# Kernel tuning notes

Hardware: AMD Instinct MI355X
Metric: run time of the kernel (lower is better)

The kernel has to match this reference:

```python
import jax, jax.numpy as jnp
import numpy as np

B, T, IN, H = 131072, 10, 1, 32


def setup_inputs() -> dict:
    key = jax.random.key(0)
    ks = jax.random.split(key, 8)
    s = 1.0 / np.sqrt(H)  # torch default uniform bound 1/sqrt(hidden)
    return {
        "x": jax.random.normal(ks[0], (B, T, IN), dtype=jnp.float32),
        "h_state": jnp.zeros((1, B, H), dtype=jnp.float32),
        "W_ih": jax.random.uniform(ks[1], (H, IN), jnp.float32, -s, s),
        "W_hh": jax.random.uniform(ks[2], (H, H), jnp.float32, -s, s),
        "b_ih": jax.random.uniform(ks[3], (H,), jnp.float32, -s, s),
        "b_hh": jax.random.uniform(ks[4], (H,), jnp.float32, -s, s),
        "W_out": jax.random.uniform(ks[5], (1, H), jnp.float32, -s, s),
        "b_out": jax.random.uniform(ks[6], (1,), jnp.float32, -s, s),
    }


def reference(x, h_state, W_ih, W_hh, b_ih, b_hh, W_out, b_out):
    # single-layer tanh RNN, batch_first; h_state: [1, B, H]
    h0 = h_state[0]  # [B, H]
    xs = jnp.swapaxes(x, 0, 1)  # [T, B, IN]

    def step(h, xt):
        h_new = jnp.tanh(xt @ W_ih.T + b_ih + h @ W_hh.T + b_hh)
        return h_new, h_new

    hT, hs = jax.lax.scan(step, h0, xs)  # hs: [T, B, H]
    r_out = jnp.swapaxes(hs, 0, 1)  # [B, T, H]
    outs = r_out @ W_out.T + b_out  # [B, T, 1] (same as view(-1,32)->Linear->view)
    return outs, hT[None]
```

## Files before the change

kernel.cpp:

```cpp
#include <hip/hip_runtime.h>

typedef __attribute__((ext_vector_type(4))) float f32x4;
typedef __attribute__((ext_vector_type(8))) short s16x8;
typedef __attribute__((ext_vector_type(4))) int   i32x4;

constexpr int BATCH = 131072;
constexpr int T = 10;
constexpr int H = 32;

__device__ __forceinline__ unsigned cvt_pk_bf16(float a, float b) {
    unsigned d;
    asm("v_cvt_pk_bf16_f32 %0, %1, %2" : "=v"(d) : "v"(a), "v"(b));
    return d;
}

__device__ __forceinline__ void pack_hilo8(const float (&v)[8], i32x4& hi, i32x4& lo) {
    #pragma unroll
    for (int p = 0; p < 4; ++p) {
        unsigned hb = cvt_pk_bf16(v[2*p], v[2*p+1]);
        float f0 = __builtin_bit_cast(float, hb << 16);
        float f1 = __builtin_bit_cast(float, hb & 0xFFFF0000u);
        hi[p] = (int)hb;
        lo[p] = (int)cvt_pk_bf16(v[2*p] - f0, v[2*p+1] - f1);
    }
}

__device__ __forceinline__ i32x4 pack_hi8(const float (&v)[8]) {
    i32x4 hi;
    #pragma unroll
    for (int p = 0; p < 4; ++p)
        hi[p] = (int)cvt_pk_bf16(v[2*p], v[2*p+1]);
    return hi;
}

__device__ __forceinline__ f32x4 mfma16(i32x4 a, i32x4 b, f32x4 c) {
    return __builtin_amdgcn_mfma_f32_16x16x32_bf16(
        __builtin_bit_cast(s16x8, a), __builtin_bit_cast(s16x8, b), c, 0, 0, 0);
}

__device__ __forceinline__ float fast_tanh(float v) {
    float e = __expf(2.0f * v);
    return fmaf(-2.0f, __builtin_amdgcn_rcpf(e + 1.0f), 1.0f);
}


extern "C" __global__ void __launch_bounds__(256, 4)
rnn_mfma(const float* __restrict__ x,
         const float* __restrict__ h0,
         const float* __restrict__ W_ih,
         const float* __restrict__ W_hh,
         const float* __restrict__ b_ih,
         const float* __restrict__ b_hh,
         const float* __restrict__ W_out,
         const float* __restrict__ b_out,
         float* __restrict__ out)
{
    const int tid  = threadIdx.x;
    const int wave = tid >> 6;
    const int lane = tid & 63;
    const int nl   = lane & 15;
    const int g    = lane >> 4;
    const int base = blockIdx.x * 128 + wave * 32;
    const int m0   = base + nl;
    const int m1   = base + 16 + nl;

    i32x4 a0h, a0l, a1h, a1l;
    {
        float v[8];
        const float* r0 = W_hh + nl * H;
        float4 u0 = *reinterpret_cast<const float4*>(r0 + 4 * g);
        float4 u1 = *reinterpret_cast<const float4*>(r0 + 16 + 4 * g);
        v[0]=u0.x; v[1]=u0.y; v[2]=u0.z; v[3]=u0.w;
        v[4]=u1.x; v[5]=u1.y; v[6]=u1.z; v[7]=u1.w;
        pack_hilo8(v, a0h, a0l);
        const float* r1 = W_hh + (nl + 16) * H;
        float4 w0 = *reinterpret_cast<const float4*>(r1 + 4 * g);
        float4 w1 = *reinterpret_cast<const float4*>(r1 + 16 + 4 * g);
        v[0]=w0.x; v[1]=w0.y; v[2]=w0.z; v[3]=w0.w;
        v[4]=w1.x; v[5]=w1.y; v[6]=w1.z; v[7]=w1.w;
        pack_hilo8(v, a1h, a1l);
    }

    float vb0[4], vw0[4], wo0[4], vb1[4], vw1[4], wo1[4];
    #pragma unroll
    for (int r = 0; r < 4; ++r) {
        const int j0 = 4 * g + r, j1 = j0 + 16;
        vb0[r] = b_ih[j0] + b_hh[j0]; vw0[r] = W_ih[j0]; wo0[r] = W_out[j0];
        vb1[r] = b_ih[j1] + b_hh[j1]; vw1[r] = W_ih[j1]; wo1[r] = W_out[j1];
    }
    const float bo = b_out[0];

    i32x4 bh[2];
    #pragma unroll
    for (int u = 0; u < 2; ++u) {
        float v[8];
        const float* hr = h0 + (size_t)((u == 0) ? m0 : m1) * H;
        float4 u0 = *reinterpret_cast<const float4*>(hr + 4 * g);
        float4 u1 = *reinterpret_cast<const float4*>(hr + 16 + 4 * g);
        v[0]=u0.x; v[1]=u0.y; v[2]=u0.z; v[3]=u0.w;
        v[4]=u1.x; v[5]=u1.y; v[6]=u1.z; v[7]=u1.w;
        bh[u] = pack_hi8(v);
    }

    const float* xr0 = x + (size_t)m0 * T;
    const float* xr1 = x + (size_t)m1 * T;

    float hc0[2][4], hc1[2][4];
    float xt0 = xr0[0], xt1 = xr1[0];

    #pragma unroll 1
    for (int t = 0; t < T; ++t) {
        float xn0 = (t + 1 < T) ? xr0[t + 1] : 0.0f;
        float xn1 = (t + 1 < T) ? xr1[t + 1] : 0.0f;

        f32x4 d0[2], d1[2];
        #pragma unroll
        for (int r = 0; r < 4; ++r) {
            d0[0][r] = fmaf(xt0, vw0[r], vb0[r]);
            d1[0][r] = fmaf(xt0, vw1[r], vb1[r]);
            d0[1][r] = fmaf(xt1, vw0[r], vb0[r]);
            d1[1][r] = fmaf(xt1, vw1[r], vb1[r]);
        }

        #pragma unroll
        for (int u = 0; u < 2; ++u) { d0[u] = mfma16(a0h, bh[u], d0[u]);
                                      d1[u] = mfma16(a1h, bh[u], d1[u]); }
        #pragma unroll
        for (int u = 0; u < 2; ++u) { d0[u] = mfma16(a0l, bh[u], d0[u]);
                                      d1[u] = mfma16(a1l, bh[u], d1[u]); }

        #pragma unroll
        for (int u = 0; u < 2; ++u) {
            float o = 0.0f;
            #pragma unroll
            for (int r = 0; r < 4; ++r) {
                hc0[u][r] = fast_tanh(d0[u][r]);
                hc1[u][r] = fast_tanh(d1[u][r]);
                o = fmaf(hc0[u][r], wo0[r], o);
                o = fmaf(hc1[u][r], wo1[r], o);
            }
            o += __shfl_xor(o, 32);
            o += __shfl_xor(o, 16);
            if (g == 0) out[(size_t)(base + u * 16 + nl) * T + t] = o + bo;

            if (t + 1 < T) {
                bh[u] = (i32x4){(int)cvt_pk_bf16(hc0[u][0], hc0[u][1]),
                                (int)cvt_pk_bf16(hc0[u][2], hc0[u][3]),
                                (int)cvt_pk_bf16(hc1[u][0], hc1[u][1]),
                                (int)cvt_pk_bf16(hc1[u][2], hc1[u][3])};
            }
        }
        xt0 = xn0;
        xt1 = xn1;
    }

    #pragma unroll
    for (int u = 0; u < 2; ++u) {
        float* hb = out + (size_t)BATCH * T + (size_t)(base + u * 16 + nl) * H;
        float4 s0, s1;
        s0.x = hc0[u][0]; s0.y = hc0[u][1]; s0.z = hc0[u][2]; s0.w = hc0[u][3];
        s1.x = hc1[u][0]; s1.y = hc1[u][1]; s1.z = hc1[u][2]; s1.w = hc1[u][3];
        *reinterpret_cast<float4*>(hb + 4 * g)      = s0;
        *reinterpret_cast<float4*>(hb + 16 + 4 * g) = s1;
    }
}

extern "C" void kernel_launch(void* const* d_in, const int* in_sizes, int n_in,
                              void* d_out, int out_size, void* d_ws, size_t ws_size,
                              hipStream_t stream) {
    const float* x     = (const float*)d_in[0];
    const float* h0    = (const float*)d_in[1];
    const float* W_ih  = (const float*)d_in[2];
    const float* W_hh  = (const float*)d_in[3];
    const float* b_ih  = (const float*)d_in[4];
    const float* b_hh  = (const float*)d_in[5];
    const float* W_out = (const float*)d_in[6];
    const float* b_out = (const float*)d_in[7];
    float* out = (float*)d_out;

    rnn_mfma<<<BATCH / 128, 256, 0, stream>>>(
        x, h0, W_ih, W_hh, b_ih, b_hh, W_out, b_out, out);
}
```

Baseline: 27.92 us.

## Halve per-wave batch tile and compute output projection with MFMA

Each wave now handles 16 batch rows instead of 32, the grid doubles, and the launch bound raises the occupancy target from 4 to 8 blocks. The per-step output projection (W_out dot h) moves from scalar FMAs plus two cross-lane shuffles onto an extra MFMA, using a W_out operand that is zero except in lane group nl==0. This cuts register pressure and shuffle work and adds more waves to hide latency. In exchange it loses the two independent MFMA chains per wave that overlapped each other, and the output now uses bf16-rounded h and W_out, which lowers precision.

Result: faster. 27.07 us (-3.0%).

```diff
diff --git a/kernel.cpp b/kernel.cpp
--- a/kernel.cpp
+++ b/kernel.cpp
@@ -44,7 +44,7 @@
 }
 
 
-extern "C" __global__ void __launch_bounds__(256, 4)
+extern "C" __global__ void __launch_bounds__(256, 8)
 rnn_mfma(const float* __restrict__ x,
          const float* __restrict__ h0,
          const float* __restrict__ W_ih,
@@ -60,9 +60,7 @@
     const int lane = tid & 63;
     const int nl   = lane & 15;
     const int g    = lane >> 4;
-    const int base = blockIdx.x * 128 + wave * 32;
-    const int m0   = base + nl;
-    const int m1   = base + 16 + nl;
+    const int m    = blockIdx.x * 64 + wave * 16 + nl;
 
     i32x4 a0h, a0l, a1h, a1l;
     {
@@ -81,88 +79,83 @@
         pack_hilo8(v, a1h, a1l);
     }
 
-    float vb0[4], vw0[4], wo0[4], vb1[4], vw1[4], wo1[4];
+    i32x4 aout;
+    {
+        float v[8];
+        float4 u0 = *reinterpret_cast<const float4*>(W_out + 4 * g);
+        float4 u1 = *reinterpret_cast<const float4*>(W_out + 16 + 4 * g);
+        v[0]=u0.x; v[1]=u0.y; v[2]=u0.z; v[3]=u0.w;
+        v[4]=u1.x; v[5]=u1.y; v[6]=u1.z; v[7]=u1.w;
+        i32x4 tw = pack_hi8(v);
+        aout = (nl == 0) ? tw : (i32x4){0, 0, 0, 0};
+    }
+
+    float vb0[4], vw0[4], vb1[4], vw1[4];
     #pragma unroll
     for (int r = 0; r < 4; ++r) {
         const int j0 = 4 * g + r, j1 = j0 + 16;
-        vb0[r] = b_ih[j0] + b_hh[j0]; vw0[r] = W_ih[j0]; wo0[r] = W_out[j0];
-        vb1[r] = b_ih[j1] + b_hh[j1]; vw1[r] = W_ih[j1]; wo1[r] = W_out[j1];
+        vb0[r] = b_ih[j0] + b_hh[j0]; vw0[r] = W_ih[j0];
+        vb1[r] = b_ih[j1] + b_hh[j1]; vw1[r] = W_ih[j1];
     }
     const float bo = b_out[0];
 
-    i32x4 bh[2];
-    #pragma unroll
-    for (int u = 0; u < 2; ++u) {
+    i32x4 bh;
+    {
         float v[8];
-        const float* hr = h0 + (size_t)((u == 0) ? m0 : m1) * H;
+        const float* hr = h0 + (size_t)m * H;
         float4 u0 = *reinterpret_cast<const float4*>(hr + 4 * g);
         float4 u1 = *reinterpret_cast<const float4*>(hr + 16 + 4 * g);
         v[0]=u0.x; v[1]=u0.y; v[2]=u0.z; v[3]=u0.w;
         v[4]=u1.x; v[5]=u1.y; v[6]=u1.z; v[7]=u1.w;
-        bh[u] = pack_hi8(v);
+        bh = pack_hi8(v);
     }
 
-    const float* xr0 = x + (size_t)m0 * T;
-    const float* xr1 = x + (size_t)m1 * T;
+    const float* xr   = x + (size_t)m * T;
+    float*       orow = out + (size_t)m * T;
 
-    float hc0[2][4], hc1[2][4];
-    float xt0 = xr0[0], xt1 = xr1[0];
+    f32x4 d0, d1;
+    float xt = xr[0];
 
     #pragma unroll 1
     for (int t = 0; t < T; ++t) {
-        float xn0 = (t + 1 < T) ? xr0[t + 1] : 0.0f;
-        float xn1 = (t + 1 < T) ? xr1[t + 1] : 0.0f;
+        float xn = (t + 1 < T) ? xr[t + 1] : 0.0f;
 
-        f32x4 d0[2], d1[2];
+        f32x4 c0, c1;
         #pragma unroll
         for (int r = 0; r < 4; ++r) {
-            d0[0][r] = fmaf(xt0, vw0[r], vb0[r]);
-            d1[0][r] = fmaf(xt0, vw1[r], vb1[r]);
-            d0[1][r] = fmaf(xt1, vw0[r], vb0[r]);
-            d1[1][r] = fmaf(xt1, vw1[r], vb1[r]);
+            c0[r] = fmaf(xt, vw0[r], vb0[r]);
+            c1[r] = fmaf(xt, vw1[r], vb1[r]);
         }
 
-        #pragma unroll
-        for (int u = 0; u < 2; ++u) { d0[u] = mfma16(a0h, bh[u], d0[u]);
-                                      d1[u] = mfma16(a1h, bh[u], d1[u]); }
-        #pragma unroll
-        for (int u = 0; u < 2; ++u) { d0[u] = mfma16(a0l, bh[u], d0[u]);
-                                      d1[u] = mfma16(a1l, bh[u], d1[u]); }
+        c0 = mfma16(a0h, bh, c0);
+        c1 = mfma16(a1h, bh, c1);
+        c0 = mfma16(a0l, bh, c0);
+        c1 = mfma16(a1l, bh, c1);
 
         #pragma unroll
-        for (int u = 0; u < 2; ++u) {
-            float o = 0.0f;
-            #pragma unroll
-            for (int r = 0; r < 4; ++r) {
-                hc0[u][r] = fast_tanh(d0[u][r]);
-                hc1[u][r] = fast_tanh(d1[u][r]);
-                o = fmaf(hc0[u][r], wo0[r], o);
-                o = fmaf(hc1[u][r], wo1[r], o);
-            }
-            o += __shfl_xor(o, 32);
-            o += __shfl_xor(o, 16);
-            if (g == 0) out[(size_t)(base + u * 16 + nl) * T + t] = o + bo;
+        for (int r = 0; r < 4; ++r) {
+            d0[r] = fast_tanh(c0[r]);
+            d1[r] = fast_tanh(c1[r]);
+        }
 
-            if (t + 1 < T) {
-                bh[u] = (i32x4){(int)cvt_pk_bf16(hc0[u][0], hc0[u][1]),
-                                (int)cvt_pk_bf16(hc0[u][2], hc0[u][3]),
-                                (int)cvt_pk_bf16(hc1[u][0], hc1[u][1]),
-                                (int)cvt_pk_bf16(hc1[u][2], hc1[u][3])};
-            }
-        }
-        xt0 = xn0;
-        xt1 = xn1;
+        bh = (i32x4){(int)cvt_pk_bf16(d0[0], d0[1]),
+                     (int)cvt_pk_bf16(d0[2], d0[3]),
+                     (int)cvt_pk_bf16(d1[0], d1[1]),
+                     (int)cvt_pk_bf16(d1[2], d1[3])};
+
+        f32x4 oacc = {0.0f, 0.0f, 0.0f, 0.0f};
+        oacc = mfma16(aout, bh, oacc);
+        if (g == 0) orow[t] = oacc[0] + bo;
+
+        xt = xn;
     }
 
-    #pragma unroll
-    for (int u = 0; u < 2; ++u) {
-        float* hb = out + (size_t)BATCH * T + (size_t)(base + u * 16 + nl) * H;
-        float4 s0, s1;
-        s0.x = hc0[u][0]; s0.y = hc0[u][1]; s0.z = hc0[u][2]; s0.w = hc0[u][3];
-        s1.x = hc1[u][0]; s1.y = hc1[u][1]; s1.z = hc1[u][2]; s1.w = hc1[u][3];
-        *reinterpret_cast<float4*>(hb + 4 * g)      = s0;
-        *reinterpret_cast<float4*>(hb + 16 + 4 * g) = s1;
-    }
+    float* hb = out + (size_t)BATCH * T + (size_t)m * H;
+    float4 s0, s1;
+    s0.x = d0[0]; s0.y = d0[1]; s0.z = d0[2]; s0.w = d0[3];
+    s1.x = d1[0]; s1.y = d1[1]; s1.z = d1[2]; s1.w = d1[3];
+    *reinterpret_cast<float4*>(hb + 4 * g)      = s0;
+    *reinterpret_cast<float4*>(hb + 16 + 4 * g) = s1;
 }
 
 extern "C" void kernel_launch(void* const* d_in, const int* in_sizes, int n_in,
@@ -178,6 +171,6 @@
     const float* b_out = (const float*)d_in[7];
     float* out = (float*)d_out;
 
-    rnn_mfma<<<BATCH / 128, 256, 0, stream>>>(
+    rnn_mfma<<<BATCH / 64, 256, 0, stream>>>(
         x, h0, W_ih, W_hh, b_ih, b_hh, W_out, b_out, out);
 }
```

## Compute output projection with MFMA and preload x row into registers

Applied to the files above, without the earlier changes.

The output projection (h · W_out) moves from per-lane FMAs plus two cross-lane shuffles to one bf16 MFMA per half-tile, using a W_out A-operand that is zero except in row 0. The bf16-packed hidden state is reused as the B operand. The whole x row is loaded up front as float2 vectors instead of being fetched per timestep. This removes shuffles and per-step scalar loads, but lowers output precision (bf16 h, hi part only of W_out) and adds MFMA latency plus extra registers.

Result: faster. 24.59 us (-11.9%).

```diff
diff --git a/kernel.cpp b/kernel.cpp
--- a/kernel.cpp
+++ b/kernel.cpp
@@ -81,12 +81,23 @@
         pack_hilo8(v, a1h, a1l);
     }
 
-    float vb0[4], vw0[4], wo0[4], vb1[4], vw1[4], wo1[4];
+    i32x4 aout;
+    {
+        float v[8];
+        float4 u0 = *reinterpret_cast<const float4*>(W_out + 4 * g);
+        float4 u1 = *reinterpret_cast<const float4*>(W_out + 16 + 4 * g);
+        v[0]=u0.x; v[1]=u0.y; v[2]=u0.z; v[3]=u0.w;
+        v[4]=u1.x; v[5]=u1.y; v[6]=u1.z; v[7]=u1.w;
+        i32x4 tw = pack_hi8(v);
+        aout = (nl == 0) ? tw : (i32x4){0, 0, 0, 0};
+    }
+
+    float vb0[4], vw0[4], vb1[4], vw1[4];
     #pragma unroll
     for (int r = 0; r < 4; ++r) {
         const int j0 = 4 * g + r, j1 = j0 + 16;
-        vb0[r] = b_ih[j0] + b_hh[j0]; vw0[r] = W_ih[j0]; wo0[r] = W_out[j0];
-        vb1[r] = b_ih[j1] + b_hh[j1]; vw1[r] = W_ih[j1]; wo1[r] = W_out[j1];
+        vb0[r] = b_ih[j0] + b_hh[j0]; vw0[r] = W_ih[j0];
+        vb1[r] = b_ih[j1] + b_hh[j1]; vw1[r] = W_ih[j1];
     }
     const float bo = b_out[0];
 
@@ -102,64 +113,62 @@
         bh[u] = pack_hi8(v);
     }
 
-    const float* xr0 = x + (size_t)m0 * T;
-    const float* xr1 = x + (size_t)m1 * T;
+    float xv[2][T];
+    {
+        const float2* p0 = reinterpret_cast<const float2*>(x + (size_t)m0 * T);
+        const float2* p1 = reinterpret_cast<const float2*>(x + (size_t)m1 * T);
+        #pragma unroll
+        for (int i = 0; i < T / 2; ++i) {
+            float2 a = p0[i]; xv[0][2*i] = a.x; xv[0][2*i+1] = a.y;
+            float2 b = p1[i]; xv[1][2*i] = b.x; xv[1][2*i+1] = b.y;
+        }
+    }
 
-    float hc0[2][4], hc1[2][4];
-    float xt0 = xr0[0], xt1 = xr1[0];
+    f32x4 d0[2], d1[2];
 
     #pragma unroll 1
     for (int t = 0; t < T; ++t) {
-        float xn0 = (t + 1 < T) ? xr0[t + 1] : 0.0f;
-        float xn1 = (t + 1 < T) ? xr1[t + 1] : 0.0f;
+        const float xt0 = xv[0][t], xt1 = xv[1][t];
 
-        f32x4 d0[2], d1[2];
+        f32x4 c0[2], c1[2];
         #pragma unroll
         for (int r = 0; r < 4; ++r) {
-            d0[0][r] = fmaf(xt0, vw0[r], vb0[r]);
-            d1[0][r] = fmaf(xt0, vw1[r], vb1[r]);
-            d0[1][r] = fmaf(xt1, vw0[r], vb0[r]);
-            d1[1][r] = fmaf(xt1, vw1[r], vb1[r]);
+            c0[0][r] = fmaf(xt0, vw0[r], vb0[r]);
+            c1[0][r] = fmaf(xt0, vw1[r], vb1[r]);
+            c0[1][r] = fmaf(xt1, vw0[r], vb0[r]);
+            c1[1][r] = fmaf(xt1, vw1[r], vb1[r]);
         }
 
         #pragma unroll
-        for (int u = 0; u < 2; ++u) { d0[u] = mfma16(a0h, bh[u], d0[u]);
-                                      d1[u] = mfma16(a1h, bh[u], d1[u]); }
+        for (int u = 0; u < 2; ++u) { c0[u] = mfma16(a0h, bh[u], c0[u]);
+                                      c1[u] = mfma16(a1h, bh[u], c1[u]); }
         #pragma unroll
-        for (int u = 0; u < 2; ++u) { d0[u] = mfma16(a0l, bh[u], d0[u]);
-                                      d1[u] = mfma16(a1l, bh[u], d1[u]); }
+        for (int u = 0; u < 2; ++u) { c0[u] = mfma16(a0l, bh[u], c0[u]);
+                                      c1[u] = mfma16(a1l, bh[u], c1[u]); }
 
         #pragma unroll
         for (int u = 0; u < 2; ++u) {
-            float o = 0.0f;
             #pragma unroll
             for (int r = 0; r < 4; ++r) {
-                hc0[u][r] = fast_tanh(d0[u][r]);
-                hc1[u][r] = fast_tanh(d1[u][r]);
-                o = fmaf(hc0[u][r], wo0[r], o);
-                o = fmaf(hc1[u][r], wo1[r], o);
+                d0[u][r] = fast_tanh(c0[u][r]);
+                d1[u][r] = fast_tanh(c1[u][r]);
             }
-            o += __shfl_xor(o, 32);
-            o += __shfl_xor(o, 16);
-            if (g == 0) out[(size_t)(base + u * 16 + nl) * T + t] = o + bo;
-
-            if (t + 1 < T) {
-                bh[u] = (i32x4){(int)cvt_pk_bf16(hc0[u][0], hc0[u][1]),
-                                (int)cvt_pk_bf16(hc0[u][2], hc0[u][3]),
-                                (int)cvt_pk_bf16(hc1[u][0], hc1[u][1]),
-                                (int)cvt_pk_bf16(hc1[u][2], hc1[u][3])};
-            }
+            bh[u] = (i32x4){(int)cvt_pk_bf16(d0[u][0], d0[u][1]),
+                            (int)cvt_pk_bf16(d0[u][2], d0[u][3]),
+                            (int)cvt_pk_bf16(d1[u][0], d1[u][1]),
+                            (int)cvt_pk_bf16(d1[u][2], d1[u][3])};
+            f32x4 oacc = {0.0f, 0.0f, 0.0f, 0.0f};
+            oacc = mfma16(aout, bh[u], oacc);
+            if (g == 0) out[(size_t)(base + u * 16 + nl) * T + t] = oacc[0] + bo;
         }
-        xt0 = xn0;
-        xt1 = xn1;
     }
 
     #pragma unroll
     for (int u = 0; u < 2; ++u) {
         float* hb = out + (size_t)BATCH * T + (size_t)(base + u * 16 + nl) * H;
         float4 s0, s1;
-        s0.x = hc0[u][0]; s0.y = hc0[u][1]; s0.z = hc0[u][2]; s0.w = hc0[u][3];
-        s1.x = hc1[u][0]; s1.y = hc1[u][1]; s1.z = hc1[u][2]; s1.w = hc1[u][3];
+        s0.x = d0[u][0]; s0.y = d0[u][1]; s0.z = d0[u][2]; s0.w = d0[u][3];
+        s1.x = d1[u][0]; s1.y = d1[u][1]; s1.z = d1[u][2]; s1.w = d1[u][3];
         *reinterpret_cast<float4*>(hb + 4 * g)      = s0;
         *reinterpret_cast<float4*>(hb + 16 + 4 * g) = s1;
     }
```
